# Kernel tuning notes

Measured on AMD Instinct MI355X. Metric: run time of the kernel, lower is better.

The kernel has to match this reference:

```python
import jax, jax.numpy as jnp
import numpy as np

B, C, H, W = 32, 256, 112, 112
ROI, SCALE, MAX_GRID, HID = 7, 0.25, 4, 1152
IMG = 448  # image-space extent (feats are stride-4, spatial_scale=0.25)


def setup_inputs() -> dict:
    key = jax.random.key(0)
    ks = jax.random.split(key, 8)
    feats = jax.random.normal(ks[0], (B, C, H, W), jnp.float32)
    # boxes in image coords, side length in [32,112] px so adaptive grid <= MAX_GRID
    x1 = jax.random.uniform(ks[1], (B,), minval=0.0, maxval=IMG - 120.0)
    y1 = jax.random.uniform(ks[2], (B,), minval=0.0, maxval=IMG - 120.0)
    bw = jax.random.uniform(ks[3], (B,), minval=32.0, maxval=112.0)
    bh = jax.random.uniform(ks[4], (B,), minval=32.0, maxval=112.0)
    boxes_xyxy = jnp.stack([x1, y1, x1 + bw, y1 + bh], axis=1)
    fan_in = C * ROI * ROI  # 12544
    W_proj = jax.random.normal(ks[5], (fan_in, HID), jnp.float32) / np.float32(np.sqrt(fan_in))
    b_proj = jnp.zeros((HID,), jnp.float32)
    ln_gamma = jnp.ones((HID,), jnp.float32)
    ln_beta = jnp.zeros((HID,), jnp.float32)
    sign_cls = jnp.zeros((1, 1, HID), jnp.float32)
    return dict(feats=feats, boxes_xyxy=boxes_xyxy, W_proj=W_proj, b_proj=b_proj,
                ln_gamma=ln_gamma, ln_beta=ln_beta, sign_cls=sign_cls)


def _roi_align_one(feat, box):
    # feat [C,Hc,Wc]; box [4] xyxy in image coords. torchvision roi_align with
    # aligned=True, sampling_ratio=-1 (adaptive, statically capped at MAX_GRID via masking).
    Hc, Wc = feat.shape[1], feat.shape[2]
    sx = box[0] * SCALE - 0.5
    sy = box[1] * SCALE - 0.5
    ex = box[2] * SCALE - 0.5
    ey = box[3] * SCALE - 0.5
    roi_w, roi_h = ex - sx, ey - sy
    bin_w, bin_h = roi_w / ROI, roi_h / ROI
    gw = jnp.clip(jnp.ceil(roi_w / ROI), 1.0, float(MAX_GRID))  # adaptive grid size
    gh = jnp.clip(jnp.ceil(roi_h / ROI), 1.0, float(MAX_GRID))
    p = jnp.arange(ROI, dtype=feat.dtype)
    g = jnp.arange(MAX_GRID, dtype=feat.dtype)
    ys = (sy + p[:, None] * bin_h + (g[None, :] + 0.5) * bin_h / gh).reshape(-1)  # [ROI*MAX_GRID]
    xs = (sx + p[:, None] * bin_w + (g[None, :] + 0.5) * bin_w / gw).reshape(-1)
    my = jnp.broadcast_to(g[None, :] < gh, (ROI, MAX_GRID)).reshape(-1)
    mx = jnp.broadcast_to(g[None, :] < gw, (ROI, MAX_GRID)).reshape(-1)

    def axis(v, n, m):
        valid = (v >= -1.0) & (v <= n) & m
        vc = jnp.clip(v, 0.0, n - 1.0)
        i0 = jnp.clip(jnp.floor(vc), 0, n - 2).astype(jnp.int32)
        return i0, i0 + 1, vc - i0, valid

    y0, y1, ly, vy = axis(ys, Hc, my)
    x0, x1, lx, vx = axis(xs, Wc, mx)
    hy, hx = 1.0 - ly, 1.0 - lx
    # bilinear gather over all sample points: [C, NY, NX]
    v = (feat[:, y0[:, None], x0[None, :]] * (hy[:, None] * hx[None, :])
         + feat[:, y0[:, None], x1[None, :]] * (hy[:, None] * lx[None, :])
         + feat[:, y1[:, None], x0[None, :]] * (ly[:, None] * hx[None, :])
         + feat[:, y1[:, None], x1[None, :]] * (ly[:, None] * lx[None, :]))
    v = v * (vy[:, None] & vx[None, :])
    v = v.reshape(feat.shape[0], ROI, MAX_GRID, ROI, MAX_GRID)
    return v.sum(axis=(2, 4)) / (gh * gw)  # [C, ROI, ROI]


def reference(feats, boxes_xyxy, W_proj, b_proj, ln_gamma, ln_beta, sign_cls):
    pooled = jax.vmap(_roi_align_one)(feats, boxes_xyxy)          # [B, C, ROI, ROI]
    x = pooled.reshape(pooled.shape[0], -1)                       # [B, C*ROI*ROI]
    h = x @ W_proj + b_proj                                       # [B, HID]
    mu = h.mean(axis=-1, keepdims=True)
    var = ((h - mu) ** 2).mean(axis=-1, keepdims=True)
    tok = ln_gamma * (h - mu) * jax.lax.rsqrt(var + 1e-5) + ln_beta
    cls = jnp.broadcast_to(sign_cls, (feats.shape[0], 1, sign_cls.shape[-1]))
    return jnp.concatenate([cls, tok[:, None, :]], axis=1)        # [B, 2, HID]
```

## Files before the change

kernel.cpp:

```cpp
#include <hip/hip_runtime.h>

#define NB 32
#define NC 256
#define HC 112
#define WC 112
#define ROI 7
#define KTOT 12544
#define HID 1152
#define NCK 64
#define CK 196
#define BN 128
#define FSCALE 0.25f

__global__ __launch_bounds__(256) void roi_align_kernel(
    const float* __restrict__ feats, const float* __restrict__ boxes,
    float* __restrict__ xout) {
  int idx = blockIdx.x * 256 + threadIdx.x;
  int b   = idx / KTOT;
  int rem = idx - b * KTOT;
  int c   = rem / 49;
  int bin = rem - c * 49;
  int py  = bin / 7;
  int px  = bin - py * 7;

  float bx0 = boxes[b * 4 + 0], by0 = boxes[b * 4 + 1];
  float bx1 = boxes[b * 4 + 2], by1 = boxes[b * 4 + 3];
  float sx = bx0 * FSCALE - 0.5f;
  float sy = by0 * FSCALE - 0.5f;
  float ex = bx1 * FSCALE - 0.5f;
  float ey = by1 * FSCALE - 0.5f;
  float roi_w = ex - sx, roi_h = ey - sy;
  float bin_w = roi_w / 7.0f, bin_h = roi_h / 7.0f;
  float gwf = ceilf(roi_w / 7.0f); gwf = fminf(fmaxf(gwf, 1.0f), 4.0f);
  float ghf = ceilf(roi_h / 7.0f); ghf = fminf(fmaxf(ghf, 1.0f), 4.0f);
  int igw = (int)gwf, igh = (int)ghf;

  const float* fp = feats + (size_t)(b * NC + c) * (HC * WC);
  float acc = 0.0f;
  for (int gy = 0; gy < igh; ++gy) {
    float y = sy + (float)py * bin_h + ((float)gy + 0.5f) * bin_h / ghf;
    bool vy = (y >= -1.0f) && (y <= (float)HC);
    float yc = fminf(fmaxf(y, 0.0f), (float)(HC - 1));
    int y0 = (int)floorf(yc); if (y0 > HC - 2) y0 = HC - 2;
    float ly = yc - (float)y0;
    float hy = 1.0f - ly;
    const float* r0 = fp + y0 * WC;
    const float* r1 = r0 + WC;
    for (int gx = 0; gx < igw; ++gx) {
      float x = sx + (float)px * bin_w + ((float)gx + 0.5f) * bin_w / gwf;
      bool vx = (x >= -1.0f) && (x <= (float)WC);
      if (vy && vx) {
        float xc = fminf(fmaxf(x, 0.0f), (float)(WC - 1));
        int x0 = (int)floorf(xc); if (x0 > WC - 2) x0 = WC - 2;
        float lx = xc - (float)x0;
        float hx = 1.0f - lx;
        float v = r0[x0]     * (hy * hx) + r0[x0 + 1] * (hy * lx)
                + r1[x0]     * (ly * hx) + r1[x0 + 1] * (ly * lx);
        acc += v;
      }
    }
  }
  xout[idx] = acc / (ghf * gwf);
}

__global__ __launch_bounds__(BN) void proj_partial_kernel(
    const float* __restrict__ x, const float* __restrict__ Wp,
    float* __restrict__ hbuf) {
  int nb = blockIdx.x % (HID / BN);
  int ck = blockIdx.x / (HID / BN);
  int n  = nb * BN + threadIdx.x;
  int k0 = ck * CK;

  __shared__ float xs[NB][CK];
  for (int i = threadIdx.x; i < NB * CK; i += BN) {
    int b  = i / CK;
    int kk = i - b * CK;
    xs[b][kk] = x[b * KTOT + k0 + kk];
  }
  __syncthreads();

  float acc[NB];
#pragma unroll
  for (int b = 0; b < NB; ++b) acc[b] = 0.0f;

  const float* wp = Wp + (size_t)k0 * HID + n;
  for (int kk = 0; kk < CK; kk += 4) {
    float w0 = wp[(size_t)(kk + 0) * HID];
    float w1 = wp[(size_t)(kk + 1) * HID];
    float w2 = wp[(size_t)(kk + 2) * HID];
    float w3 = wp[(size_t)(kk + 3) * HID];
#pragma unroll
    for (int b = 0; b < NB; ++b) {
      float4 xv = *(const float4*)&xs[b][kk];
      acc[b] = fmaf(xv.x, w0, acc[b]);
      acc[b] = fmaf(xv.y, w1, acc[b]);
      acc[b] = fmaf(xv.z, w2, acc[b]);
      acc[b] = fmaf(xv.w, w3, acc[b]);
    }
  }

#pragma unroll
  for (int b = 0; b < NB; ++b)
    atomicAdd(&hbuf[(size_t)b * HID + n], acc[b]);
}

__global__ __launch_bounds__(256) void finish_kernel(
    const float* __restrict__ hbuf, const float* __restrict__ bias,
    const float* __restrict__ gamma, const float* __restrict__ beta,
    const float* __restrict__ cls, float* __restrict__ out) {
  int b = blockIdx.x;
  __shared__ float hrow[HID];
  __shared__ float rs[4], rq[4];

  float lsum = 0.0f, lsq = 0.0f;
  for (int n = threadIdx.x; n < HID; n += 256) {
    float s = bias[n] + hbuf[(size_t)b * HID + n];
    hrow[n] = s;
    lsum += s;
    lsq  += s * s;
  }
  for (int off = 32; off > 0; off >>= 1) {
    lsum += __shfl_down(lsum, off, 64);
    lsq  += __shfl_down(lsq,  off, 64);
  }
  int wid  = threadIdx.x >> 6;
  int lane = threadIdx.x & 63;
  if (lane == 0) { rs[wid] = lsum; rq[wid] = lsq; }
  __syncthreads();
  if (threadIdx.x == 0) {
    float s = 0.0f, q = 0.0f;
#pragma unroll
    for (int i = 0; i < 4; ++i) { s += rs[i]; q += rq[i]; }
    rs[0] = s; rq[0] = q;
  }
  __syncthreads();
  float mu  = rs[0] * (1.0f / HID);
  float var = rq[0] * (1.0f / HID) - mu * mu;
  float rstd = rsqrtf(var + 1e-5f);

  float* ob = out + (size_t)b * 2 * HID;
  for (int n = threadIdx.x; n < HID; n += 256) {
    ob[n] = cls[n];
    ob[HID + n] = gamma[n] * (hrow[n] - mu) * rstd + beta[n];
  }
}

extern "C" void kernel_launch(void* const* d_in, const int* in_sizes, int n_in,
                              void* d_out, int out_size, void* d_ws, size_t ws_size,
                              hipStream_t stream) {
  const float* feats = (const float*)d_in[0];
  const float* boxes = (const float*)d_in[1];
  const float* Wp    = (const float*)d_in[2];
  const float* bias  = (const float*)d_in[3];
  const float* gamma = (const float*)d_in[4];
  const float* beta  = (const float*)d_in[5];
  const float* cls   = (const float*)d_in[6];
  float* out = (float*)d_out;

  float* xbuf = (float*)d_ws;
  float* hbuf = (float*)((char*)d_ws + (size_t)NB * KTOT * 4);

  hipMemsetAsync(hbuf, 0, (size_t)NB * HID * 4, stream);
  roi_align_kernel<<<(NB * KTOT) / 256, 256, 0, stream>>>(feats, boxes, xbuf);
  proj_partial_kernel<<<(HID / BN) * NCK, BN, 0, stream>>>(xbuf, Wp, hbuf);
  finish_kernel<<<NB, 256, 0, stream>>>(hbuf, bias, gamma, beta, cls, out);
}
```

Before: 561.3 us.

## Unroll ROI-align sampling with precomputed weights and restructure projection K-split

After: 548.7 us. 2.2% less time.

```diff
diff --git a/kernel.cpp b/kernel.cpp
--- a/kernel.cpp
+++ b/kernel.cpp
@@ -4,12 +4,10 @@
 #define NC 256
 #define HC 112
 #define WC 112
-#define ROI 7
 #define KTOT 12544
 #define HID 1152
-#define NCK 64
-#define CK 196
-#define BN 128
+#define NCK 112
+#define CK 112
 #define FSCALE 0.25f
 
 __global__ __launch_bounds__(256) void roi_align_kernel(
@@ -23,75 +21,83 @@
   int py  = bin / 7;
   int px  = bin - py * 7;
 
-  float bx0 = boxes[b * 4 + 0], by0 = boxes[b * 4 + 1];
-  float bx1 = boxes[b * 4 + 2], by1 = boxes[b * 4 + 3];
-  float sx = bx0 * FSCALE - 0.5f;
-  float sy = by0 * FSCALE - 0.5f;
-  float ex = bx1 * FSCALE - 0.5f;
-  float ey = by1 * FSCALE - 0.5f;
-  float roi_w = ex - sx, roi_h = ey - sy;
-  float bin_w = roi_w / 7.0f, bin_h = roi_h / 7.0f;
-  float gwf = ceilf(roi_w / 7.0f); gwf = fminf(fmaxf(gwf, 1.0f), 4.0f);
-  float ghf = ceilf(roi_h / 7.0f); ghf = fminf(fmaxf(ghf, 1.0f), 4.0f);
-  int igw = (int)gwf, igh = (int)ghf;
+  float4 bx = ((const float4*)boxes)[b];
+  float sx = bx.x * FSCALE - 0.5f;
+  float sy = bx.y * FSCALE - 0.5f;
+  float roi_w = bx.z * FSCALE - 0.5f - sx;
+  float roi_h = bx.w * FSCALE - 0.5f - sy;
+  float bin_w = roi_w * (1.0f / 7.0f);
+  float bin_h = roi_h * (1.0f / 7.0f);
+  float gwf = fminf(fmaxf(ceilf(bin_w), 1.0f), 4.0f);
+  float ghf = fminf(fmaxf(ceilf(bin_h), 1.0f), 4.0f);
+
+  float y_base = sy + (float)py * bin_h;
+  float x_base = sx + (float)px * bin_w;
+  float step_y = bin_h / ghf, step_x = bin_w / gwf;
+
+  int   ry0[4], rx0[4];
+  float why[4], wly[4], whx[4], wlx[4];
+#pragma unroll
+  for (int g = 0; g < 4; ++g) {
+    float y  = y_base + ((float)g + 0.5f) * step_y;
+    float vy = ((float)g < ghf && y >= -1.0f && y <= (float)HC) ? 1.0f : 0.0f;
+    float yc = fminf(fmaxf(y, 0.0f), (float)(HC - 1));
+    int   y0 = (int)yc; if (y0 > HC - 2) y0 = HC - 2;
+    float ly = yc - (float)y0;
+    ry0[g] = y0; wly[g] = ly * vy; why[g] = (1.0f - ly) * vy;
+
+    float x  = x_base + ((float)g + 0.5f) * step_x;
+    float vx = ((float)g < gwf && x >= -1.0f && x <= (float)WC) ? 1.0f : 0.0f;
+    float xc = fminf(fmaxf(x, 0.0f), (float)(WC - 1));
+    int   x0 = (int)xc; if (x0 > WC - 2) x0 = WC - 2;
+    float lx = xc - (float)x0;
+    rx0[g] = x0; wlx[g] = lx * vx; whx[g] = (1.0f - lx) * vx;
+  }
 
   const float* fp = feats + (size_t)(b * NC + c) * (HC * WC);
   float acc = 0.0f;
-  for (int gy = 0; gy < igh; ++gy) {
-    float y = sy + (float)py * bin_h + ((float)gy + 0.5f) * bin_h / ghf;
-    bool vy = (y >= -1.0f) && (y <= (float)HC);
-    float yc = fminf(fmaxf(y, 0.0f), (float)(HC - 1));
-    int y0 = (int)floorf(yc); if (y0 > HC - 2) y0 = HC - 2;
-    float ly = yc - (float)y0;
-    float hy = 1.0f - ly;
-    const float* r0 = fp + y0 * WC;
+#pragma unroll
+  for (int gy = 0; gy < 4; ++gy) {
+    const float* r0 = fp + ry0[gy] * WC;
     const float* r1 = r0 + WC;
-    for (int gx = 0; gx < igw; ++gx) {
-      float x = sx + (float)px * bin_w + ((float)gx + 0.5f) * bin_w / gwf;
-      bool vx = (x >= -1.0f) && (x <= (float)WC);
-      if (vy && vx) {
-        float xc = fminf(fmaxf(x, 0.0f), (float)(WC - 1));
-        int x0 = (int)floorf(xc); if (x0 > WC - 2) x0 = WC - 2;
-        float lx = xc - (float)x0;
-        float hx = 1.0f - lx;
-        float v = r0[x0]     * (hy * hx) + r0[x0 + 1] * (hy * lx)
-                + r1[x0]     * (ly * hx) + r1[x0 + 1] * (ly * lx);
-        acc += v;
-      }
+    float hy = why[gy], ly = wly[gy];
+#pragma unroll
+    for (int gx = 0; gx < 4; ++gx) {
+      int x0 = rx0[gx];
+      float f00 = r0[x0], f01 = r0[x0 + 1];
+      float f10 = r1[x0], f11 = r1[x0 + 1];
+      acc = fmaf(hy * whx[gx], f00, acc);
+      acc = fmaf(hy * wlx[gx], f01, acc);
+      acc = fmaf(ly * whx[gx], f10, acc);
+      acc = fmaf(ly * wlx[gx], f11, acc);
     }
   }
   xout[idx] = acc / (ghf * gwf);
 }
 
-__global__ __launch_bounds__(BN) void proj_partial_kernel(
+__global__ __launch_bounds__(128) void proj_kernel(
     const float* __restrict__ x, const float* __restrict__ Wp,
     float* __restrict__ hbuf) {
-  int nb = blockIdx.x % (HID / BN);
-  int ck = blockIdx.x / (HID / BN);
-  int n  = nb * BN + threadIdx.x;
+  int nb = blockIdx.x % 9;
+  int ck = blockIdx.x / 9;
+  int n  = nb * 128 + threadIdx.x;
   int k0 = ck * CK;
-
-  __shared__ float xs[NB][CK];
-  for (int i = threadIdx.x; i < NB * CK; i += BN) {
-    int b  = i / CK;
-    int kk = i - b * CK;
-    xs[b][kk] = x[b * KTOT + k0 + kk];
-  }
-  __syncthreads();
 
   float acc[NB];
 #pragma unroll
   for (int b = 0; b < NB; ++b) acc[b] = 0.0f;
 
   const float* wp = Wp + (size_t)k0 * HID + n;
+  const float* xp = x + k0;
   for (int kk = 0; kk < CK; kk += 4) {
-    float w0 = wp[(size_t)(kk + 0) * HID];
-    float w1 = wp[(size_t)(kk + 1) * HID];
-    float w2 = wp[(size_t)(kk + 2) * HID];
-    float w3 = wp[(size_t)(kk + 3) * HID];
+    float w0 = wp[0 * HID];
+    float w1 = wp[1 * HID];
+    float w2 = wp[2 * HID];
+    float w3 = wp[3 * HID];
+    wp += 4 * HID;
 #pragma unroll
     for (int b = 0; b < NB; ++b) {
-      float4 xv = *(const float4*)&xs[b][kk];
+      float4 xv = *(const float4*)(xp + (size_t)b * KTOT + kk);
       acc[b] = fmaf(xv.x, w0, acc[b]);
       acc[b] = fmaf(xv.y, w1, acc[b]);
       acc[b] = fmaf(xv.z, w2, acc[b]);
@@ -162,6 +168,6 @@
 
   hipMemsetAsync(hbuf, 0, (size_t)NB * HID * 4, stream);
   roi_align_kernel<<<(NB * KTOT) / 256, 256, 0, stream>>>(feats, boxes, xbuf);
-  proj_partial_kernel<<<(HID / BN) * NCK, BN, 0, stream>>>(xbuf, Wp, hbuf);
+  proj_kernel<<<9 * NCK, 128, 0, stream>>>(xbuf, Wp, hbuf);
   finish_kernel<<<NB, 256, 0, stream>>>(hbuf, bias, gamma, beta, cls, out);
 }
```
